# Optimization experiments

Measured on AMD Instinct MI355X. Metric: run time of the kernel, lower is better.

Reference implementation:

```python
import jax, jax.numpy as jnp
import numpy as np

B, S, D, H = 2, 2048, 1024, 16
HD = D // H  # head_dim = 64


def setup_inputs() -> dict:
    key = jax.random.key(0)
    ks = jax.random.split(key, 5)
    scale = 0.02
    x = jax.random.normal(ks[0], (B, S, D), dtype=jnp.float32)
    Wq = scale * jax.random.normal(ks[1], (H, D, HD), dtype=jnp.float32)
    Wk = scale * jax.random.normal(ks[2], (H, D, HD), dtype=jnp.float32)
    Wv = scale * jax.random.normal(ks[3], (H, D, HD), dtype=jnp.float32)
    Wo = scale * jax.random.normal(ks[4], (D, D), dtype=jnp.float32)
    bq = jnp.zeros((H, HD), dtype=jnp.float32)
    bk = jnp.zeros((H, HD), dtype=jnp.float32)
    bv = jnp.zeros((H, HD), dtype=jnp.float32)
    bo = jnp.zeros((D,), dtype=jnp.float32)
    return {"x": x, "Wq": Wq, "bq": bq, "Wk": Wk, "bk": bk,
            "Wv": Wv, "bv": bv, "Wo": Wo, "bo": bo}


def reference(x, Wq, bq, Wk, bk, Wv, bv, Wo, bo):
    # Per-head QKV projections (the torch module's per-head nn.Linear list,
    # vectorized over the head axis h). Dropout is identity (eval mode).
    q = jnp.einsum("bsd,hde->bhse", x, Wq) + bq[None, :, None, :]  # [B,H,S,HD]
    k = jnp.einsum("bsd,hde->bhse", x, Wk) + bk[None, :, None, :]
    v = jnp.einsum("bsd,hde->bhse", x, Wv) + bv[None, :, None, :]

    norm = jnp.asarray(np.sqrt(HD), dtype=x.dtype)
    scores = jnp.einsum("bhse,bhte->bhst", q, k) / norm  # [B,H,S,S]
    causal = jnp.tril(jnp.ones((S, S), dtype=bool))
    scores = jnp.where(causal[None, None], scores, jnp.asarray(-jnp.inf, dtype=scores.dtype))
    attn = jax.nn.softmax(scores, axis=-1)

    wv = jnp.einsum("bhst,bhte->bhse", attn, v)          # [B,H,S,HD]
    wv = jnp.transpose(wv, (0, 2, 1, 3)).reshape(B, S, D)  # concat heads on last dim
    out = wv @ Wo.T + bo                                   # output projection
    return out
```

## Files before the change

kernel.cpp:

```cpp
#include <hip/hip_runtime.h>


#define DD 1024
#define SS 2048
#define BB 2
#define HH 16
#define HD 64
#define QSCALE 0.18033688011112042f
#define LSTR 88

typedef __attribute__((ext_vector_type(8))) short short8;
typedef __attribute__((ext_vector_type(4))) float float4v;
typedef unsigned short ushort;
typedef unsigned int uint;

__device__ inline ushort f2bf(float f) {
    union { float f; uint i; } v; v.f = f;
    uint r = v.i + 0x7FFF + ((v.i >> 16) & 1);
    return (ushort)(r >> 16);
}
#if __has_builtin(__builtin_amdgcn_cvt_pk_bf16_f32)
typedef __bf16 bf16x2 __attribute__((ext_vector_type(2)));
__device__ inline uint pack_bf2(float a, float b) {
    union { bf16x2 v; uint u; } c;
    c.v = __builtin_amdgcn_cvt_pk_bf16_f32(a, b);
    return c.u;
}
#else
__device__ inline uint pack_bf2(float a, float b) {
    union { float f; uint i; } x, y; x.f = a; y.f = b;
    return ((x.i + 0x8000u) >> 16) | (((y.i + 0x8000u) >> 16) << 16);
}
#endif

__device__ __forceinline__ void cp16(const ushort* g, ushort* l) {
    __builtin_amdgcn_global_load_lds((const __attribute__((address_space(1))) void*)g,
                                     (__attribute__((address_space(3))) void*)l,
                                     16, 0, 0);
}

__global__ __launch_bounds__(256) void prep(const float* __restrict__ x,
                                            const float* __restrict__ Wo,
                                            const float* __restrict__ Wq,
                                            const float* __restrict__ Wk,
                                            const float* __restrict__ Wv,
                                            ushort* __restrict__ xb,
                                            ushort* __restrict__ Wob,
                                            ushort* __restrict__ W3T) {
    __shared__ ushort T[64][65];
    int bid = blockIdx.x, t = threadIdx.x;
    if (bid < 5120) {
        const float* src; ushort* dst; int j;
        if (bid < 4096) { src = x;  dst = xb;  j = bid * 256 + t; }
        else            { src = Wo; dst = Wob; j = (bid - 4096) * 256 + t; }
        float4 v = ((const float4*)src)[j];
        ushort o[4] = { f2bf(v.x), f2bf(v.y), f2bf(v.z), f2bf(v.w) };
        ((uint2*)dst)[j] = *(const uint2*)o;
        return;
    }
    int i = bid - 5120;
    int z = i >> 8, h = (i >> 4) & 15, d0 = (i & 15) * 64;
    const float* W = z == 0 ? Wq : (z == 1 ? Wk : Wv);
    const float* Wh = W + h * DD * HD;
    ushort* Wt = W3T + ((size_t)z * HH + h) * HD * DD;
    #pragma unroll
    for (int s = 0; s < 4; s++) {
        int idx = t + s * 256;
        int d = idx >> 4, e4 = (idx & 15) * 4;
        float4 v = *(const float4*)(Wh + (d0 + d) * HD + e4);
        T[d][e4 + 0] = f2bf(v.x); T[d][e4 + 1] = f2bf(v.y);
        T[d][e4 + 2] = f2bf(v.z); T[d][e4 + 3] = f2bf(v.w);
    }
    __syncthreads();
    #pragma unroll
    for (int s = 0; s < 2; s++) {
        int idx = t + s * 256;
        int e = idx >> 3, d8 = (idx & 7) * 8;
        ushort tmp[8];
        #pragma unroll
        for (int j = 0; j < 8; j++) tmp[j] = T[d8 + j][e];
        *(uint4*)(Wt + e * DD + d0 + d8) = *(uint4*)tmp;
    }
}

__global__ __launch_bounds__(256) void gemm_qkv(const ushort* __restrict__ xb,
                                                const ushort* __restrict__ W3T,
                                                const float* __restrict__ bq,
                                                const float* __restrict__ bk,
                                                const float* __restrict__ bv,
                                                ushort* __restrict__ qb,
                                                ushort* __restrict__ kb,
                                                ushort* __restrict__ vT) {
    __shared__ ushort Al[128 * 64];
    __shared__ ushort Bl[3][64 * 64];
    int m0 = blockIdx.x * 128, n0 = blockIdx.y * 64;
    int t = threadIdx.x, lane = t & 63, w = t >> 6;
    int wm = w & 1, wn = w >> 1;
    int qm = lane >> 4, lm = lane & 15;

    const ushort* W0 = W3T + (size_t)n0 * DD;
    const ushort* W1 = W3T + (size_t)(HH * HD + n0) * DD;
    const ushort* W2 = W3T + (size_t)(2 * HH * HD + n0) * DD;

    float4v acc[3][4][2] = {};
    for (int k0 = 0; k0 < DD; k0 += 64) {
        __syncthreads();
        #pragma unroll
        for (int s = 0; s < 4; s++) {
            int c = t + s * 256;
            int row = c >> 3;
            int j = (c & 7) ^ (row & 7);
            cp16(xb + (size_t)(m0 + row) * DD + k0 + j * 8, Al + c * 8);
        }
        #pragma unroll
        for (int s = 0; s < 2; s++) {
            int c = t + s * 256;
            int row = c >> 3;
            int j = (c & 7) ^ (row & 7);
            cp16(W0 + (size_t)row * DD + k0 + j * 8, Bl[0] + c * 8);
            cp16(W1 + (size_t)row * DD + k0 + j * 8, Bl[1] + c * 8);
            cp16(W2 + (size_t)row * DD + k0 + j * 8, Bl[2] + c * 8);
        }
        __syncthreads();
        #pragma unroll
        for (int h2 = 0; h2 < 2; h2++) {
            int sw = ((((h2 << 2) | qm) ^ (lm & 7)) << 3);
            short8 a[4];
            #pragma unroll
            for (int i = 0; i < 4; i++)
                a[i] = *(const short8*)(Al + ((wm * 64 + i * 16 + lm) << 6) + sw);
            #pragma unroll
            for (int z = 0; z < 3; z++) {
                short8 b0 = *(const short8*)(Bl[z] + ((wn * 32 + lm) << 6) + sw);
                short8 b1 = *(const short8*)(Bl[z] + ((wn * 32 + 16 + lm) << 6) + sw);
                if (z == 2) {
                    #pragma unroll
                    for (int i = 0; i < 4; i++) {
                        acc[2][i][0] = __builtin_amdgcn_mfma_f32_16x16x32_bf16(a[i], b0, acc[2][i][0], 0, 0, 0);
                        acc[2][i][1] = __builtin_amdgcn_mfma_f32_16x16x32_bf16(a[i], b1, acc[2][i][1], 0, 0, 0);
                    }
                } else {
                    #pragma unroll
                    for (int i = 0; i < 4; i++) {
                        acc[z][i][0] = __builtin_amdgcn_mfma_f32_16x16x32_bf16(b0, a[i], acc[z][i][0], 0, 0, 0);
                        acc[z][i][1] = __builtin_amdgcn_mfma_f32_16x16x32_bf16(b1, a[i], acc[z][i][1], 0, 0, 0);
                    }
                }
            }
        }
    }
    #pragma unroll
    for (int z = 0; z < 2; z++) {
        const float* bias = z == 0 ? bq : bk;
        ushort* Out = z == 0 ? qb : kb;
        float sc = z == 0 ? QSCALE : 1.0f;
        #pragma unroll
        for (int j = 0; j < 2; j++) {
            int nb = n0 + wn * 32 + j * 16 + qm * 4;
            float4 b4 = *(const float4*)(bias + nb);
            #pragma unroll
            for (int i = 0; i < 4; i++) {
                int m = m0 + wm * 64 + i * 16 + lm;
                uint2 o2;
                o2.x = pack_bf2((acc[z][i][j][0] + b4.x) * sc, (acc[z][i][j][1] + b4.y) * sc);
                o2.y = pack_bf2((acc[z][i][j][2] + b4.z) * sc, (acc[z][i][j][3] + b4.w) * sc);
                *(uint2*)(Out + (size_t)m * DD + nb) = o2;
            }
        }
    }
    #pragma unroll
    for (int j = 0; j < 2; j++) {
        int n = n0 + wn * 32 + j * 16 + lm;
        int h = n >> 6, e = n & 63;
        float bb = bv[n];
        #pragma unroll
        for (int i = 0; i < 4; i++) {
            int m = m0 + wm * 64 + i * 16 + qm * 4;
            int b_ = m >> 11, s = m & (SS - 1);
            uint2 o2;
            o2.x = pack_bf2(acc[2][i][j][0] + bb, acc[2][i][j][1] + bb);
            o2.y = pack_bf2(acc[2][i][j][2] + bb, acc[2][i][j][3] + bb);
            *(uint2*)(vT + ((size_t)(b_ * HH + h) * HD + e) * SS + s) = o2;
        }
    }
}

__global__ __launch_bounds__(512, 4) void attn(const ushort* __restrict__ Q,
                                               const ushort* __restrict__ K,
                                               const ushort* __restrict__ VT,
                                               ushort* __restrict__ O) {
    __shared__ ushort QP[128][LSTR];
    __shared__ ushort Kl[2][64 * 64];
    __shared__ ushort Vl[2][64 * 64];
    int id = blockIdx.x;
    int bh = id & 31;
    int j5 = (id >> 5) & 7;
    int qt = (id < 256) ? (15 - 2 * j5) : (2 * j5);
    int b = bh >> 4, h = bh & 15;
    int m0 = qt * 128;
    int njt = 2 * (qt + 1);
    const ushort* Qp = Q + (size_t)b * SS * DD + h * HD;
    const ushort* Kp = K + (size_t)b * SS * DD + h * HD;
    const ushort* Vp = VT + (size_t)bh * HD * SS;
    int t = threadIdx.x, lane = t & 63, w = t >> 6;
    int qm = lane >> 4, lm = lane & 15;
    int row0 = t >> 3, colc = (t & 7) * 8;
    int srow = t >> 3;
    int sj = (t & 7) ^ (srow & 7);

    *(uint4*)(&QP[row0][colc])      = *(const uint4*)(Qp + (size_t)(m0 + row0) * DD + colc);
    *(uint4*)(&QP[row0 + 64][colc]) = *(const uint4*)(Qp + (size_t)(m0 + row0 + 64) * DD + colc);
    cp16(Kp + (size_t)srow * DD + sj * 8, Kl[0] + t * 8);
    cp16(Vp + (size_t)srow * SS + sj * 8, Vl[0] + t * 8);
    __syncthreads();

    short8 qf[2];
    qf[0] = *(const short8*)(&QP[w * 16 + lm][qm * 8]);
    qf[1] = *(const short8*)(&QP[w * 16 + lm][32 + qm * 8]);

    float4v o[4] = {};
    float li = 0.f;
    int cur = 0;
    int qg = m0 + w * 16 + lm;
    int swz = ((qm ^ (lm & 7)) << 3);
    int swz1 = (((4 | qm) ^ (lm & 7)) << 3);

    for (int jt = 0; jt < njt; jt++) {
        if (jt) __syncthreads();
        if (jt + 1 < njt) {
            int nn = (jt + 1) * 64;
            cp16(Kp + (size_t)(nn + srow) * DD + sj * 8, Kl[cur ^ 1] + t * 8);
            cp16(Vp + (size_t)srow * SS + nn + sj * 8, Vl[cur ^ 1] + t * 8);
        }

        float4v s[4] = {};
        #pragma unroll
        for (int j = 0; j < 4; j++) {
            short8 ak0 = *(const short8*)(Kl[cur] + ((j * 16 + lm) << 6) + swz);
            short8 ak1 = *(const short8*)(Kl[cur] + ((j * 16 + lm) << 6) + swz1);
            s[j] = __builtin_amdgcn_mfma_f32_16x16x32_bf16(ak0, qf[0], s[j], 0, 0, 0);
            s[j] = __builtin_amdgcn_mfma_f32_16x16x32_bf16(ak1, qf[1], s[j], 0, 0, 0);
        }
        if (jt >= 2 * qt) {
            #pragma unroll
            for (int j = 0; j < 4; j++)
                #pragma unroll
                for (int r = 0; r < 4; r++)
                    if (jt * 64 + j * 16 + qm * 4 + r > qg) s[j][r] = -__builtin_inff();
        }
        #pragma unroll
        for (int j = 0; j < 4; j++) {
            float p0 = __builtin_amdgcn_exp2f(s[j][0]);
            float p1 = __builtin_amdgcn_exp2f(s[j][1]);
            float p2 = __builtin_amdgcn_exp2f(s[j][2]);
            float p3 = __builtin_amdgcn_exp2f(s[j][3]);
            li += (p0 + p1) + (p2 + p3);
            uint2 u; u.x = pack_bf2(p0, p1); u.y = pack_bf2(p2, p3);
            *(uint2*)(&QP[w * 16 + lm][j * 16 + qm * 4]) = u;
        }
        asm volatile("s_waitcnt lgkmcnt(0)" ::: "memory");

        #pragma unroll
        for (int kc = 0; kc < 2; kc++) {
            short8 ap = *(const short8*)(&QP[w * 16 + lm][kc * 32 + qm * 8]);
            int so = kc ? swz1 : swz;
            #pragma unroll
            for (int jn = 0; jn < 4; jn++) {
                short8 av = *(const short8*)(Vl[cur] + ((jn * 16 + lm) << 6) + so);
                o[jn] = __builtin_amdgcn_mfma_f32_16x16x32_bf16(av, ap, o[jn], 0, 0, 0);
            }
        }
        cur ^= 1;
    }
    li += __shfl_xor(li, 16, 64);
    li += __shfl_xor(li, 32, 64);
    float inv = 1.f / li;
    ushort* Ob = O + ((size_t)b * SS + qg) * DD + h * HD;
    #pragma unroll
    for (int jn = 0; jn < 4; jn++) {
        uint2 u;
        u.x = pack_bf2(o[jn][0] * inv, o[jn][1] * inv);
        u.y = pack_bf2(o[jn][2] * inv, o[jn][3] * inv);
        *(uint2*)(Ob + jn * 16 + qm * 4) = u;
    }
}

__global__ __launch_bounds__(256) void gemm_out(const ushort* __restrict__ X,
                                                const ushort* __restrict__ Wob,
                                                const float* __restrict__ bo,
                                                float* __restrict__ Out) {
    __shared__ ushort Al[128 * 64];
    __shared__ ushort Bl[64 * 64];
    int m0 = blockIdx.x * 128, n0 = blockIdx.y * 64;
    int t = threadIdx.x, lane = t & 63, w = t >> 6;
    int wm = w & 1, wn = w >> 1;
    int qm = lane >> 4, lm = lane & 15;

    float4v acc[4][2] = {};
    for (int k0 = 0; k0 < DD; k0 += 64) {
        __syncthreads();
        #pragma unroll
        for (int s = 0; s < 4; s++) {
            int c = t + s * 256;
            int row = c >> 3;
            int j = (c & 7) ^ (row & 7);
            cp16(X + (size_t)(m0 + row) * DD + k0 + j * 8, Al + c * 8);
        }
        #pragma unroll
        for (int s = 0; s < 2; s++) {
            int c = t + s * 256;
            int row = c >> 3;
            int j = (c & 7) ^ (row & 7);
            cp16(Wob + (size_t)(n0 + row) * DD + k0 + j * 8, Bl + c * 8);
        }
        __syncthreads();
        #pragma unroll
        for (int h2 = 0; h2 < 2; h2++) {
            int sw = ((((h2 << 2) | qm) ^ (lm & 7)) << 3);
            short8 a[4], b[2];
            #pragma unroll
            for (int i = 0; i < 4; i++)
                a[i] = *(const short8*)(Al + ((wm * 64 + i * 16 + lm) << 6) + sw);
            #pragma unroll
            for (int j = 0; j < 2; j++)
                b[j] = *(const short8*)(Bl + ((wn * 32 + j * 16 + lm) << 6) + sw);
            #pragma unroll
            for (int i = 0; i < 4; i++)
                #pragma unroll
                for (int j = 0; j < 2; j++)
                    acc[i][j] = __builtin_amdgcn_mfma_f32_16x16x32_bf16(b[j], a[i], acc[i][j], 0, 0, 0);
        }
    }
    #pragma unroll
    for (int j = 0; j < 2; j++) {
        int nb = n0 + wn * 32 + j * 16 + qm * 4;
        float4 b4 = *(const float4*)(bo + nb);
        #pragma unroll
        for (int i = 0; i < 4; i++) {
            int m = m0 + wm * 64 + i * 16 + lm;
            float4 st;
            st.x = acc[i][j][0] + b4.x;
            st.y = acc[i][j][1] + b4.y;
            st.z = acc[i][j][2] + b4.z;
            st.w = acc[i][j][3] + b4.w;
            *(float4*)(Out + (size_t)m * DD + nb) = st;
        }
    }
}

extern "C" void kernel_launch(void* const* d_in, const int* in_sizes, int n_in,
                              void* d_out, int out_size, void* d_ws, size_t ws_size,
                              hipStream_t stream) {
    const float* x   = (const float*)d_in[0];
    const float* Wq  = (const float*)d_in[1];
    const float* bq  = (const float*)d_in[2];
    const float* Wk  = (const float*)d_in[3];
    const float* bk  = (const float*)d_in[4];
    const float* Wv_ = (const float*)d_in[5];
    const float* bv  = (const float*)d_in[6];
    const float* Wo  = (const float*)d_in[7];
    const float* bo  = (const float*)d_in[8];
    float* out = (float*)d_out;

    ushort* xb  = (ushort*)d_ws;
    ushort* W3T = xb  + (size_t)BB * SS * DD;
    ushort* Wob = W3T + (size_t)3 * HH * HD * DD;
    ushort* qb  = Wob + (size_t)DD * DD;
    ushort* kb  = qb + (size_t)BB * SS * DD;
    ushort* vT  = kb + (size_t)BB * SS * DD;
    ushort* wvb = vT + (size_t)BB * SS * DD;

    prep<<<dim3(5888), 256, 0, stream>>>(x, Wo, Wq, Wk, Wv_, xb, Wob, W3T);
    gemm_qkv<<<dim3(32, 16), 256, 0, stream>>>(xb, W3T, bq, bk, bv, qb, kb, vT);
    attn<<<dim3(512), 512, 0, stream>>>(qb, kb, vT, wvb);
    gemm_out<<<dim3(32, 16), 256, 0, stream>>>(wvb, Wob, bo, out);
}
```

Measured before the change: 180.7 us.

## Shrink GEMM tiles to 64x64 and remap blocks per XCD for both projections

Both the QKV and output-projection GEMMs change from 128x64 tiles on a 2D grid to 64x64 tiles on a 1D grid of 1024 blocks. Each wave now computes one 16-column slice over all 64 rows. The block index is decoded so that each XCD owns a contiguous pair of N-column tiles, keeping weight tiles resident in that XCD's L2. Launch bounds now request 4 blocks per CU. The goal is more blocks to fill the 256 CUs and better L2 locality, at the cost of less data reuse per tile and more total global loads of the activation matrix.

```diff
diff --git a/kernel.cpp b/kernel.cpp
--- a/kernel.cpp
+++ b/kernel.cpp
@@ -83,40 +83,36 @@
     }
 }
 
-__global__ __launch_bounds__(256) void gemm_qkv(const ushort* __restrict__ xb,
-                                                const ushort* __restrict__ W3T,
-                                                const float* __restrict__ bq,
-                                                const float* __restrict__ bk,
-                                                const float* __restrict__ bv,
-                                                ushort* __restrict__ qb,
-                                                ushort* __restrict__ kb,
-                                                ushort* __restrict__ vT) {
-    __shared__ ushort Al[128 * 64];
+__global__ __launch_bounds__(256, 4) void gemm_qkv(const ushort* __restrict__ xb,
+                                                   const ushort* __restrict__ W3T,
+                                                   const float* __restrict__ bq,
+                                                   const float* __restrict__ bk,
+                                                   const float* __restrict__ bv,
+                                                   ushort* __restrict__ qb,
+                                                   ushort* __restrict__ kb,
+                                                   ushort* __restrict__ vT) {
+    __shared__ ushort Al[64 * 64];
     __shared__ ushort Bl[3][64 * 64];
-    int m0 = blockIdx.x * 128, n0 = blockIdx.y * 64;
+    int id = blockIdx.x;
+    int xcd = id & 7, p = id >> 3;
+    int n0 = (xcd * 2 + (p >> 6)) * 64;
+    int m0 = (p & 63) * 64;
     int t = threadIdx.x, lane = t & 63, w = t >> 6;
-    int wm = w & 1, wn = w >> 1;
     int qm = lane >> 4, lm = lane & 15;
 
     const ushort* W0 = W3T + (size_t)n0 * DD;
     const ushort* W1 = W3T + (size_t)(HH * HD + n0) * DD;
     const ushort* W2 = W3T + (size_t)(2 * HH * HD + n0) * DD;
 
-    float4v acc[3][4][2] = {};
+    float4v acc[3][4] = {};
     for (int k0 = 0; k0 < DD; k0 += 64) {
         __syncthreads();
         #pragma unroll
-        for (int s = 0; s < 4; s++) {
+        for (int s = 0; s < 2; s++) {
             int c = t + s * 256;
             int row = c >> 3;
             int j = (c & 7) ^ (row & 7);
             cp16(xb + (size_t)(m0 + row) * DD + k0 + j * 8, Al + c * 8);
-        }
-        #pragma unroll
-        for (int s = 0; s < 2; s++) {
-            int c = t + s * 256;
-            int row = c >> 3;
-            int j = (c & 7) ^ (row & 7);
             cp16(W0 + (size_t)row * DD + k0 + j * 8, Bl[0] + c * 8);
             cp16(W1 + (size_t)row * DD + k0 + j * 8, Bl[1] + c * 8);
             cp16(W2 + (size_t)row * DD + k0 + j * 8, Bl[2] + c * 8);
@@ -128,24 +124,15 @@
             short8 a[4];
             #pragma unroll
             for (int i = 0; i < 4; i++)
-                a[i] = *(const short8*)(Al + ((wm * 64 + i * 16 + lm) << 6) + sw);
-            #pragma unroll
-            for (int z = 0; z < 3; z++) {
-                short8 b0 = *(const short8*)(Bl[z] + ((wn * 32 + lm) << 6) + sw);
-                short8 b1 = *(const short8*)(Bl[z] + ((wn * 32 + 16 + lm) << 6) + sw);
-                if (z == 2) {
-                    #pragma unroll
-                    for (int i = 0; i < 4; i++) {
-                        acc[2][i][0] = __builtin_amdgcn_mfma_f32_16x16x32_bf16(a[i], b0, acc[2][i][0], 0, 0, 0);
-                        acc[2][i][1] = __builtin_amdgcn_mfma_f32_16x16x32_bf16(a[i], b1, acc[2][i][1], 0, 0, 0);
-                    }
-                } else {
-                    #pragma unroll
-                    for (int i = 0; i < 4; i++) {
-                        acc[z][i][0] = __builtin_amdgcn_mfma_f32_16x16x32_bf16(b0, a[i], acc[z][i][0], 0, 0, 0);
-                        acc[z][i][1] = __builtin_amdgcn_mfma_f32_16x16x32_bf16(b1, a[i], acc[z][i][1], 0, 0, 0);
-                    }
-                }
+                a[i] = *(const short8*)(Al + ((i * 16 + lm) << 6) + sw);
+            short8 b0 = *(const short8*)(Bl[0] + ((w * 16 + lm) << 6) + sw);
+            short8 b1 = *(const short8*)(Bl[1] + ((w * 16 + lm) << 6) + sw);
+            short8 b2 = *(const short8*)(Bl[2] + ((w * 16 + lm) << 6) + sw);
+            #pragma unroll
+            for (int i = 0; i < 4; i++) {
+                acc[0][i] = __builtin_amdgcn_mfma_f32_16x16x32_bf16(b0, a[i], acc[0][i], 0, 0, 0);
+                acc[1][i] = __builtin_amdgcn_mfma_f32_16x16x32_bf16(b1, a[i], acc[1][i], 0, 0, 0);
+                acc[2][i] = __builtin_amdgcn_mfma_f32_16x16x32_bf16(a[i], b2, acc[2][i], 0, 0, 0);
             }
         }
     }
@@ -154,32 +141,28 @@
         const float* bias = z == 0 ? bq : bk;
         ushort* Out = z == 0 ? qb : kb;
         float sc = z == 0 ? QSCALE : 1.0f;
-        #pragma unroll
-        for (int j = 0; j < 2; j++) {
-            int nb = n0 + wn * 32 + j * 16 + qm * 4;
-            float4 b4 = *(const float4*)(bias + nb);
-            #pragma unroll
-            for (int i = 0; i < 4; i++) {
-                int m = m0 + wm * 64 + i * 16 + lm;
-                uint2 o2;
-                o2.x = pack_bf2((acc[z][i][j][0] + b4.x) * sc, (acc[z][i][j][1] + b4.y) * sc);
-                o2.y = pack_bf2((acc[z][i][j][2] + b4.z) * sc, (acc[z][i][j][3] + b4.w) * sc);
-                *(uint2*)(Out + (size_t)m * DD + nb) = o2;
-            }
-        }
-    }
-    #pragma unroll
-    for (int j = 0; j < 2; j++) {
-        int n = n0 + wn * 32 + j * 16 + lm;
+        int nb = n0 + w * 16 + qm * 4;
+        float4 b4 = *(const float4*)(bias + nb);
+        #pragma unroll
+        for (int i = 0; i < 4; i++) {
+            int m = m0 + i * 16 + lm;
+            uint2 o2;
+            o2.x = pack_bf2((acc[z][i][0] + b4.x) * sc, (acc[z][i][1] + b4.y) * sc);
+            o2.y = pack_bf2((acc[z][i][2] + b4.z) * sc, (acc[z][i][3] + b4.w) * sc);
+            *(uint2*)(Out + (size_t)m * DD + nb) = o2;
+        }
+    }
+    {
+        int n = n0 + w * 16 + lm;
         int h = n >> 6, e = n & 63;
         float bb = bv[n];
         #pragma unroll
         for (int i = 0; i < 4; i++) {
-            int m = m0 + wm * 64 + i * 16 + qm * 4;
+            int m = m0 + i * 16 + qm * 4;
             int b_ = m >> 11, s = m & (SS - 1);
             uint2 o2;
-            o2.x = pack_bf2(acc[2][i][j][0] + bb, acc[2][i][j][1] + bb);
-            o2.y = pack_bf2(acc[2][i][j][2] + bb, acc[2][i][j][3] + bb);
+            o2.x = pack_bf2(acc[2][i][0] + bb, acc[2][i][1] + bb);
+            o2.y = pack_bf2(acc[2][i][2] + bb, acc[2][i][3] + bb);
             *(uint2*)(vT + ((size_t)(b_ * HH + h) * HD + e) * SS + s) = o2;
         }
     }
@@ -285,66 +268,55 @@
     }
 }
 
-__global__ __launch_bounds__(256) void gemm_out(const ushort* __restrict__ X,
-                                                const ushort* __restrict__ Wob,
-                                                const float* __restrict__ bo,
-                                                float* __restrict__ Out) {
-    __shared__ ushort Al[128 * 64];
+__global__ __launch_bounds__(256, 4) void gemm_out(const ushort* __restrict__ X,
+                                                   const ushort* __restrict__ Wob,
+                                                   const float* __restrict__ bo,
+                                                   float* __restrict__ Out) {
+    __shared__ ushort Al[64 * 64];
     __shared__ ushort Bl[64 * 64];
-    int m0 = blockIdx.x * 128, n0 = blockIdx.y * 64;
+    int id = blockIdx.x;
+    int xcd = id & 7, p = id >> 3;
+    int n0 = (xcd * 2 + (p >> 6)) * 64;
+    int m0 = (p & 63) * 64;
     int t = threadIdx.x, lane = t & 63, w = t >> 6;
-    int wm = w & 1, wn = w >> 1;
     int qm = lane >> 4, lm = lane & 15;
 
-    float4v acc[4][2] = {};
+    float4v acc[4] = {};
     for (int k0 = 0; k0 < DD; k0 += 64) {
         __syncthreads();
-        #pragma unroll
-        for (int s = 0; s < 4; s++) {
-            int c = t + s * 256;
-            int row = c >> 3;
-            int j = (c & 7) ^ (row & 7);
-            cp16(X + (size_t)(m0 + row) * DD + k0 + j * 8, Al + c * 8);
-        }
         #pragma unroll
         for (int s = 0; s < 2; s++) {
             int c = t + s * 256;
             int row = c >> 3;
             int j = (c & 7) ^ (row & 7);
+            cp16(X   + (size_t)(m0 + row) * DD + k0 + j * 8, Al + c * 8);
             cp16(Wob + (size_t)(n0 + row) * DD + k0 + j * 8, Bl + c * 8);
         }
         __syncthreads();
         #pragma unroll
         for (int h2 = 0; h2 < 2; h2++) {
             int sw = ((((h2 << 2) | qm) ^ (lm & 7)) << 3);
-            short8 a[4], b[2];
+            short8 a[4];
             #pragma unroll
             for (int i = 0; i < 4; i++)
-                a[i] = *(const short8*)(Al + ((wm * 64 + i * 16 + lm) << 6) + sw);
-            #pragma unroll
-            for (int j = 0; j < 2; j++)
-                b[j] = *(const short8*)(Bl + ((wn * 32 + j * 16 + lm) << 6) + sw);
+                a[i] = *(const short8*)(Al + ((i * 16 + lm) << 6) + sw);
+            short8 b = *(const short8*)(Bl + ((w * 16 + lm) << 6) + sw);
             #pragma unroll
             for (int i = 0; i < 4; i++)
-                #pragma unroll
-                for (int j = 0; j < 2; j++)
-                    acc[i][j] = __builtin_amdgcn_mfma_f32_16x16x32_bf16(b[j], a[i], acc[i][j], 0, 0, 0);
-        }
-    }
-    #pragma unroll
-    for (int j = 0; j < 2; j++) {
-        int nb = n0 + wn * 32 + j * 16 + qm * 4;
-        float4 b4 = *(const float4*)(bo + nb);
-        #pragma unroll
-        for (int i = 0; i < 4; i++) {
-            int m = m0 + wm * 64 + i * 16 + lm;
-            float4 st;
-            st.x = acc[i][j][0] + b4.x;
-            st.y = acc[i][j][1] + b4.y;
-            st.z = acc[i][j][2] + b4.z;
-            st.w = acc[i][j][3] + b4.w;
-            *(float4*)(Out + (size_t)m * DD + nb) = st;
-        }
+                acc[i] = __builtin_amdgcn_mfma_f32_16x16x32_bf16(b, a[i], acc[i], 0, 0, 0);
+        }
+    }
+    int nb = n0 + w * 16 + qm * 4;
+    float4 b4 = *(const float4*)(bo + nb);
+    #pragma unroll
+    for (int i = 0; i < 4; i++) {
+        int m = m0 + i * 16 + lm;
+        float4 st;
+        st.x = acc[i][0] + b4.x;
+        st.y = acc[i][1] + b4.y;
+        st.z = acc[i][2] + b4.z;
+        st.w = acc[i][3] + b4.w;
+        *(float4*)(Out + (size_t)m * DD + nb) = st;
     }
 }
 
@@ -371,7 +343,7 @@
     ushort* wvb = vT + (size_t)BB * SS * DD;
 
     prep<<<dim3(5888), 256, 0, stream>>>(x, Wo, Wq, Wk, Wv_, xb, Wob, W3T);
-    gemm_qkv<<<dim3(32, 16), 256, 0, stream>>>(xb, W3T, bq, bk, bv, qb, kb, vT);
+    gemm_qkv<<<dim3(1024), 256, 0, stream>>>(xb, W3T, bq, bk, bv, qb, kb, vT);
     attn<<<dim3(512), 512, 0, stream>>>(qb, kb, vT, wvb);
-    gemm_out<<<dim3(32, 16), 256, 0, stream>>>(wvb, Wob, bo, out);
-}
+    gemm_out<<<dim3(1024), 256, 0, stream>>>(wvb, Wob, bo, out);
+}
```

New measurement: 185.2 us. +2.5%, slower.
